# Performance work log

Hardware: AMD Instinct MI355X
Metric: run time of the kernel (lower is better)

## Reference

```python
import jax, jax.numpy as jnp
import numpy as np

B, T = 128, 1024
SERIES_IN, Y = 35, 8
H = 256
CON, BIN = 25, 10
D = SERIES_IN + Y  # 43, lstm input size


def setup_inputs() -> dict:
    key = jax.random.key(0)
    ks = jax.random.split(key, 14)
    def w(k, shape, s=0.05):
        return jax.random.normal(k, shape, dtype=jnp.float32) * s
    return {
        "x": jax.random.normal(ks[0], (B, T, D), dtype=jnp.float32),
        # DPLSTM (single layer), gate order i,f,g,o like torch
        "W_ih": w(ks[1], (4 * H, D)),
        "W_hh": w(ks[2], (4 * H, H)),
        "b_ih": w(ks[3], (4 * H,)),
        "b_hh": w(ks[4], (4 * H,)),
        # action head
        "W_afc1": w(ks[5], (H, H)),
        "b_afc1": w(ks[6], (H,)),
        "W_aout": w(ks[7], (Y, H)),
        "b_aout": w(ks[8], (Y,)),
        # outcome heads take [out, current_action] -> H+Y features
        "W_cont": w(ks[9], (2 * CON, H + Y)),
        "b_cont": w(ks[10], (2 * CON,)),
        "W_bin": w(ks[11], (BIN, H + Y)),
        "b_bin": w(ks[12], (BIN,)),
    }


def lstm(x, W_ih, W_hh, b_ih, b_hh):
    # x: [B, T, D] -> hidden states [B, T, H]; torch gate order i, f, g, o
    Hh = W_hh.shape[1]
    # precompute input projections for all timesteps (fold both biases in)
    xg = jnp.einsum("btd,gd->btg", x, W_ih) + b_ih + b_hh  # [B, T, 4H]

    def step(carry, g_t):
        h, c = carry
        gates = g_t + h @ W_hh.T  # [B, 4H]
        i, f, g, o = jnp.split(gates, 4, axis=-1)
        i = jax.nn.sigmoid(i)
        f = jax.nn.sigmoid(f)
        g = jnp.tanh(g)
        o = jax.nn.sigmoid(o)
        c = f * c + i * g
        h = o * jnp.tanh(c)
        return (h, c), h

    Bsz = x.shape[0]
    init = (jnp.zeros((Bsz, Hh), x.dtype), jnp.zeros((Bsz, Hh), x.dtype))
    _, hs = jax.lax.scan(step, init, jnp.swapaxes(xg, 0, 1))  # [T, B, H]
    return jnp.swapaxes(hs, 0, 1)


def reference(x, W_ih, W_hh, b_ih, b_hh, W_afc1, b_afc1, W_aout, b_aout,
              W_cont, b_cont, W_bin, b_bin):
    cur = x[:, :, -Y:]                                   # current action [B,T,Y]
    prev = jnp.concatenate([jnp.zeros_like(cur[:, :1]), cur[:, :-1]], axis=1)
    xin = jnp.concatenate([x[:, :, :-Y], prev], axis=-1)  # [B,T,D]
    out = lstm(xin, W_ih, W_hh, b_ih, b_hh)               # [B,T,H]
    # gradient reversal is identity in forward
    act = jax.nn.relu(out @ W_afc1.T + b_afc1) @ W_aout.T + b_aout  # [B,T,Y]
    pred = jnp.concatenate([out, cur], axis=-1)           # [B,T,H+Y]
    cont_params = pred @ W_cont.T + b_cont                # [B,T,2*CON]
    bin_params = jax.nn.sigmoid(pred @ W_bin.T + b_bin)   # [B,T,BIN]
    return cont_params, bin_params, act
```

## Files before the change

kernel.cpp:

```cpp
#include <hip/hip_runtime.h>

typedef unsigned int u32;
typedef unsigned short u16;
typedef unsigned char u8;
typedef unsigned long long u64;
typedef __attribute__((ext_vector_type(8))) short short8;
typedef __attribute__((ext_vector_type(4))) float floatx4;
typedef __attribute__((ext_vector_type(4))) int intx4;

#define TT 1024
#define BIN_OFF 6553600
#define ACT_OFF 7864320

__device__ __forceinline__ u16 f2b(float f) {
  u32 u = __builtin_bit_cast(u32, f);
  u += 0x7fffu + ((u >> 16) & 1u);
  return (u16)(u >> 16);
}
__device__ __forceinline__ float sigm2(float z) {
  return __builtin_amdgcn_rcpf(1.0f + __expf(-z));
}
__device__ __forceinline__ float tanh2(float z) {
  z = fminf(z, 15.0f);
  float e = __expf(2.0f * z);
  return (e - 1.0f) * __builtin_amdgcn_rcpf(e + 1.0f);
}
__device__ __forceinline__ float sigmf(float x) { return 1.0f / (1.0f + __expf(-x)); }


__global__ void k_zero4(u32* __restrict__ p) {
  if (threadIdx.x < 4) p[threadIdx.x] = 0;
}
__global__ void k_amax(const float* __restrict__ x, const float* __restrict__ wih,
                       const float* __restrict__ whh, u32* __restrict__ am) {
  __shared__ float red[256];
  const int tid = threadIdx.x;
  int b = blockIdx.x;
  const float* src; size_t n; int sec, b0, nb;
  if (b < 1920)      { src = x;   n = 5636096; sec = 0; b0 = 0;    nb = 1920; }
  else if (b < 2016) { src = whh; n = 262144;  sec = 1; b0 = 1920; nb = 96; }
  else               { src = wih; n = 44032;   sec = 2; b0 = 2016; nb = 32; }
  float m = 0.f;
  for (size_t i = (size_t)(b - b0) * 256 + tid; i < n; i += (size_t)nb * 256)
    m = fmaxf(m, fabsf(src[i]));
  red[tid] = m;
  __syncthreads();
  for (int s = 128; s > 0; s >>= 1) {
    if (tid < s) red[tid] = fmaxf(red[tid], red[tid + s]);
    __syncthreads();
  }
  if (tid == 0) atomicMax(&am[sec], __float_as_uint(red[0]));
}
__global__ void k_prep_bias(const float* __restrict__ a, const float* __restrict__ b,
                            float* __restrict__ o) {
  int i = blockIdx.x * 256 + threadIdx.x;
  o[i] = a[i] + b[i];
}
__global__ void k_prep_wq2(const float* __restrict__ wih, const float* __restrict__ whh,
                           const float* __restrict__ bias, const u32* __restrict__ am,
                           int* __restrict__ wq, float* __restrict__ sbuf) {
  u32 idx = blockIdx.x * 256 + threadIdx.x;
  const float xmax = fmaxf(__uint_as_float(am[0]), 1e-8f);
  const float whm  = fmaxf(__uint_as_float(am[1]), 1e-8f);
  const float wxm  = fmaxf(__uint_as_float(am[2]), 1e-8f);
  const float sn_h = whm / 127.0f, sn_x = wxm / 127.0f;
  const float sx = xmax / 127.0f;
  const float A_h = sn_h / 127.0f;
  const float A_x = sn_x * sx;
  if (idx == 0) { sbuf[0] = A_h; sbuf[1] = A_x; }
  int jq = idx & 3;
  int lane = (idx >> 2) & 63;
  u32 wf = idx >> 8;
  int F = wf % 40, w = wf / 40;
  int tile = F / 5, c = F % 5;
  int gate = tile >> 1, ht = tile & 1;
  int l15 = lane & 15, kq = lane >> 4;
  int n = gate * 256 + w * 32 + ht * 16 + l15;
  u32 out = 0;
#pragma unroll
  for (int b = 0; b < 4; ++b) {
    int kl = kq * 16 + jq * 4 + b;
    float q = 0.f;
    if (c < 4) {
      q = rintf(whh[n * 256 + c * 64 + kl] / sn_h);
    } else {
      if (kl < 43) q = rintf(wih[n * 43 + kl] / sn_x);
      else if (kl == 43) {
        q = fminf(fmaxf(rintf(bias[n] / (127.0f * A_x)), -127.f), 127.f);
      } else if (kl == 44) {
        float qc = fminf(fmaxf(rintf(bias[n] / (127.0f * A_x)), -127.f), 127.f);
        q = rintf((bias[n] - qc * 127.0f * A_x) / (127.0f * A_h));
      }
    }
    q = fminf(fmaxf(q, -127.f), 127.f);
    int qi = (int)q;
    out |= ((u32)(qi & 255)) << (8 * b);
  }
  wq[idx] = (int)out;
}
__global__ void k_prep_xq2(const float* __restrict__ x, const u32* __restrict__ am,
                           int* __restrict__ xq) {
  u32 idx = blockIdx.x * 256 + threadIdx.x;
  const float xmax = fmaxf(__uint_as_float(am[0]), 1e-8f);
  const float whm  = fmaxf(__uint_as_float(am[1]), 1e-8f);
  const float wxm  = fmaxf(__uint_as_float(am[2]), 1e-8f);
  const float sx = xmax / 127.0f;
  const float sr = whm / (127.0f * wxm);
  u32 unit = idx >> 8;
  u32 dwIn = idx & 255;
  int lane = dwIn >> 2, reg = dwIn & 3;
  int m = lane & 15, kq = lane >> 4;
  int bg = unit >> 8;
  int rem = unit & 255;
  int mt = rem >> 1, res = rem & 1;
  int t = mt * 8 + (m >> 1);
  int row = bg * 2 + (m & 1);
  u32 out = 0;
#pragma unroll
  for (int b = 0; b < 4; ++b) {
    int k = kq * 16 + reg * 4 + b;
    int q = 0;
    if (k < 43) {
      float xv = 0.f;
      if (k < 35) xv = x[((size_t)row * TT + t) * 43 + k];
      else if (t > 0) xv = x[((size_t)row * TT + (t - 1)) * 43 + k];
      float q1 = fminf(fmaxf(rintf(xv / sx), -127.f), 127.f);
      if (!res) q = (int)q1;
      else q = (int)fminf(fmaxf(rintf((xv - sx * q1) / sr), -127.f), 127.f);
    } else if (k == 43) q = res ? 0 : 127;
    else if (k == 44) q = res ? 127 : 0;
    out |= ((u32)(q & 255)) << (8 * b);
  }
  xq[idx] = (int)out;
}
__global__ void k_prep_afc(const float* __restrict__ wafc1, const float* __restrict__ waout,
                           u16* __restrict__ ob1, u16* __restrict__ ob2) {
  int r = blockIdx.x, k = threadIdx.x;
  if (r < 256) ob1[r * 256 + k] = f2b(wafc1[r * 256 + k]);
  else {
    int y = r - 256;
    ob2[y * 256 + k] = f2b(y < 8 ? waout[y * 256 + k] : 0.f);
  }
}
__global__ void k_prep_wcb(const float* __restrict__ wcont, const float* __restrict__ wbin,
                           u16* __restrict__ o) {
  int nrow = blockIdx.x, k = threadIdx.x;
  float v = 0.f;
  if (k < 264) {
    if (nrow < 50) v = wcont[nrow * 264 + k];
    else if (nrow < 60) v = wbin[(nrow - 50) * 264 + k];
  }
  o[nrow * 288 + k] = f2b(v);
}

#define XS 257
#define BARX() do { \
  asm volatile("s_waitcnt lgkmcnt(0)" ::: "memory"); \
  __builtin_amdgcn_s_barrier(); \
  __builtin_amdgcn_sched_barrier(0); \
} while (0)
#define PHASEG_HALF(xgw, HT, XM, XR) do { \
  const intx4 z_ = {0, 0, 0, 0}; \
  intx4 AX_[4], AR_[4]; \
  _Pragma("unroll") \
  for (int g_ = 0; g_ < 4; ++g_) { \
    const int F_ = (g_ * 2 + (HT)) * 5 + 4; \
    AX_[g_] = __builtin_amdgcn_mfma_i32_16x16x64_i8(wfr[F_], (XM), z_, 0, 0, 0); \
    AR_[g_] = __builtin_amdgcn_mfma_i32_16x16x64_i8(wfr[F_], (XR), z_, 0, 0, 0); \
  } \
  _Pragma("unroll") \
  for (int rr_ = 0; rr_ < 4; ++rr_) { \
    floatx4 P_; \
    _Pragma("unroll") \
    for (int g_ = 0; g_ < 4; ++g_) \
      P_[g_] = A_x * (float)AX_[g_][rr_] + A_h * (float)AR_[g_][rr_]; \
    (xgw)[l15 * XS + wcol + (HT) * 16 + rr_] = P_; \
  } \
} while (0)

__global__ __launch_bounds__(512, 1)
void k_scan12(const int* wq_, const int* __restrict__ xqd,
              const float* __restrict__ sb, u16* __restrict__ hs) {
  __shared__ u8 bimg[2 * 4096];
  __shared__ intx4 gimg[2 * XS];
  __shared__ floatx4 xg[2][16 * XS];
  const int tid = threadIdx.x;
  const int w = tid >> 6, lane = tid & 63;
  const int l15 = lane & 15, kq = lane >> 4;
  const int bg = blockIdx.x;

  *(uint4*)&bimg[tid * 16] = (uint4){0, 0, 0, 0};

  intx4 wfr[40];
  {
    const intx4* wp = (const intx4*)wq_ + (size_t)(w * 40) * 64 + lane;
#pragma unroll
    for (int F = 0; F < 40; ++F) wfr[F] = wp[(size_t)F * 64];
  }
  const float A_h = sb[0], A_x = sb[1];

  const int* xu = xqd + (size_t)bg * 65536;
  const int wcol = w * 32 + kq * 4;
  const int lr = lane >> 5, lc = lane & 31;
  const int mycol = w * 32 + lc;
  const int bwr = lr * 256 + (((mycol >> 4) ^ lr) << 4) + (mycol & 15);
  u16* hgp = hs + ((size_t)(bg * 2 + lr) * TT) * 256 + mycol;

  {
    intx4 xcm = *(const intx4*)(xu + lane * 4);
    intx4 xcr = *(const intx4*)(xu + 256 + lane * 4);
    PHASEG_HALF(xg[0], 0, xcm, xcr);
    PHASEG_HALF(xg[0], 1, xcm, xcr);
  }
  intx4 xnm = *(const intx4*)(xu + 512 + lane * 4);
  intx4 xnr = *(const intx4*)(xu + 512 + 256 + lane * 4);

  float c_st = 0.f;
  u16 h16 = 0;
  __syncthreads();

  int t = 0;
  for (int ch = 0; ch < 128; ++ch) {
    const int rb = ch & 1, wb = rb ^ 1;
#pragma unroll 1
    for (int tl = 0; tl < 8; ++tl, ++t) {
      const int cur = t & 1, nxt = cur ^ 1;
      if (t > 0) hgp[(size_t)(t - 1) * 256] = h16;
      intx4 bh[4];
#pragma unroll
      for (int c = 0; c < 4; ++c)
        bh[c] = *(const intx4*)&bimg[cur * 4096 + l15 * 256 +
                                     ((((c * 4 + kq) ^ l15) & 15) << 4)];
      floatx4 P = xg[rb][(tl * 2 + lr) * XS + mycol];
      const intx4 z = {0, 0, 0, 0};
      __builtin_amdgcn_s_setprio(1);
#pragma unroll
      for (int ht = 0; ht < 2; ++ht) {
        intx4 A[4];
#pragma unroll
        for (int g = 0; g < 4; ++g) {
          const int F = (g * 2 + ht) * 5;
          intx4 a = __builtin_amdgcn_mfma_i32_16x16x64_i8(wfr[F + 0], bh[0], z, 0, 0, 0);
          a = __builtin_amdgcn_mfma_i32_16x16x64_i8(wfr[F + 1], bh[1], a, 0, 0, 0);
          a = __builtin_amdgcn_mfma_i32_16x16x64_i8(wfr[F + 2], bh[2], a, 0, 0, 0);
          A[g] = __builtin_amdgcn_mfma_i32_16x16x64_i8(wfr[F + 3], bh[3], a, 0, 0, 0);
        }
        if (l15 < 2) {
#pragma unroll
          for (int rr = 0; rr < 4; ++rr) {
            intx4 v = {A[0][rr], A[1][rr], A[2][rr], A[3][rr]};
            gimg[l15 * XS + wcol + ht * 16 + rr] = v;
          }
        }
      }
      __builtin_amdgcn_s_setprio(0);
      asm volatile("s_waitcnt lgkmcnt(0)" ::: "memory");
      __builtin_amdgcn_sched_barrier(0);
      intx4 ah = gimg[lr * XS + mycol];
      float iv = sigm2(fmaf(A_h, (float)ah[0], P[0]));
      float fv = sigm2(fmaf(A_h, (float)ah[1], P[1]));
      float gv = tanh2(fmaf(A_h, (float)ah[2], P[2]));
      float ov = sigm2(fmaf(A_h, (float)ah[3], P[3]));
      float cc = fv * c_st + iv * gv;
      c_st = cc;
      float h = ov * tanh2(cc);
      int q = (int)rintf(h * 127.0f);
      bimg[nxt * 4096 + bwr] = (u8)q;
      h16 = f2b(h);
      if (tl == 0)      PHASEG_HALF(xg[wb], 0, xnm, xnr);
      else if (tl == 1) PHASEG_HALF(xg[wb], 1, xnm, xnr);
      else if (tl == 2) {
        const int chn = ch + 2 < 128 ? ch + 2 : 127;
        xnm = *(const intx4*)(xu + chn * 512 + lane * 4);
        xnr = *(const intx4*)(xu + chn * 512 + 256 + lane * 4);
      }
      BARX();
    }
  }
  hgp[(size_t)(TT - 1) * 256] = h16;
}


__global__ __launch_bounds__(256, 2)
void k_act(const u16* __restrict__ hs, const u16* __restrict__ wafc1,
           const u16* __restrict__ waout, const float* __restrict__ b_afc1,
           const float* __restrict__ b_aout, float* __restrict__ act) {
  __shared__ u16 a_sh[16 * 264];
  __shared__ u16 z_sh[16 * 264];
  __shared__ float sb1[256];
  const int tid = threadIdx.x;
  const int wave = tid >> 6, lane = tid & 63;
  const int l15 = lane & 15, kq = lane >> 4;
  const size_t bt0 = (size_t)blockIdx.x * 16;
  sb1[tid] = b_afc1[tid];
#pragma unroll
  for (int i = 0; i < 2; ++i) {
    int chunk = i * 256 + tid;
    int row = chunk >> 5, c = chunk & 31;
    *(uint4*)&a_sh[row * 264 + c * 8] = *(const uint4*)(hs + (bt0 + row) * 256 + c * 8);
  }
  __syncthreads();
  floatx4 acc[4];
#pragma unroll
  for (int nt = 0; nt < 4; ++nt) acc[nt] = (floatx4){0.f, 0.f, 0.f, 0.f};
#pragma unroll
  for (int kt = 0; kt < 8; ++kt) {
    short8 a = *(const short8*)&a_sh[l15 * 264 + kt * 32 + kq * 8];
#pragma unroll
    for (int nt = 0; nt < 4; ++nt) {
      int n = wave * 64 + nt * 16 + l15;
      short8 b = *(const short8*)(wafc1 + n * 256 + kt * 32 + kq * 8);
      acc[nt] = __builtin_amdgcn_mfma_f32_16x16x32_bf16(a, b, acc[nt], 0, 0, 0);
    }
  }
#pragma unroll
  for (int nt = 0; nt < 4; ++nt) {
    int n = wave * 64 + nt * 16 + l15;
    float bb = sb1[n];
#pragma unroll
    for (int r = 0; r < 4; ++r) {
      float v = acc[nt][r] + bb;
      v = v > 0.f ? v : 0.f;
      z_sh[(kq * 4 + r) * 264 + n] = f2b(v);
    }
  }
  __syncthreads();
  if (wave == 0) {
    floatx4 a2 = (floatx4){0.f, 0.f, 0.f, 0.f};
#pragma unroll
    for (int kt = 0; kt < 8; ++kt) {
      short8 a = *(const short8*)&z_sh[l15 * 264 + kt * 32 + kq * 8];
      short8 b = *(const short8*)(waout + l15 * 256 + kt * 32 + kq * 8);
      a2 = __builtin_amdgcn_mfma_f32_16x16x32_bf16(a, b, a2, 0, 0, 0);
    }
    if (l15 < 8) {
      float bb = b_aout[l15];
#pragma unroll
      for (int r = 0; r < 4; ++r)
        act[(bt0 + (size_t)(kq * 4 + r)) * 8 + l15] = a2[r] + bb;
    }
  }
}

__global__ __launch_bounds__(256, 2)
void k_cb(const u16* __restrict__ hs, const float* __restrict__ x,
          const u16* __restrict__ wcb, const float* __restrict__ b_cont,
          const float* __restrict__ b_bin, float* __restrict__ dout) {
  __shared__ u16 a_sh[16 * 296];
  const int tid = threadIdx.x;
  const int wave = tid >> 6, lane = tid & 63;
  const int l15 = lane & 15, kq = lane >> 4;
  const size_t bt0 = (size_t)blockIdx.x * 16;
#pragma unroll
  for (int i = 0; i < 2; ++i) {
    int chunk = i * 256 + tid;
    int row = chunk >> 5, c = chunk & 31;
    *(uint4*)&a_sh[row * 296 + c * 8] = *(const uint4*)(hs + (bt0 + row) * 256 + c * 8);
  }
  if (tid < 128) {
    int m = tid >> 3, j = tid & 7;
    a_sh[m * 296 + 256 + j] = f2b(x[(bt0 + m) * 43 + 35 + j]);
  }
  for (int i = tid; i < 384; i += 256) {
    int m = i / 24, jj = i % 24;
    a_sh[m * 296 + 264 + jj] = 0;
  }
  __syncthreads();
  const int n = wave * 16 + l15;
  floatx4 acc = (floatx4){0.f, 0.f, 0.f, 0.f};
#pragma unroll
  for (int kt = 0; kt < 9; ++kt) {
    short8 a = *(const short8*)&a_sh[l15 * 296 + kt * 32 + kq * 8];
    short8 b = *(const short8*)(wcb + n * 288 + kt * 32 + kq * 8);
    acc = __builtin_amdgcn_mfma_f32_16x16x32_bf16(a, b, acc, 0, 0, 0);
  }
  if (n < 50) {
    float bb = b_cont[n];
#pragma unroll
    for (int r = 0; r < 4; ++r)
      dout[(bt0 + (size_t)(kq * 4 + r)) * 50 + n] = acc[r] + bb;
  } else if (n < 60) {
    float bb = b_bin[n - 50];
#pragma unroll
    for (int r = 0; r < 4; ++r)
      dout[BIN_OFF + (bt0 + (size_t)(kq * 4 + r)) * 10 + (n - 50)] = sigmf(acc[r] + bb);
  }
}

extern "C" void kernel_launch(void* const* d_in, const int* in_sizes, int n_in,
                              void* d_out, int out_size, void* d_ws, size_t ws_size,
                              hipStream_t stream) {
  const float* x      = (const float*)d_in[0];
  const float* W_ih   = (const float*)d_in[1];
  const float* W_hh   = (const float*)d_in[2];
  const float* b_ih   = (const float*)d_in[3];
  const float* b_hh   = (const float*)d_in[4];
  const float* W_afc1 = (const float*)d_in[5];
  const float* b_afc1 = (const float*)d_in[6];
  const float* W_aout = (const float*)d_in[7];
  const float* b_aout = (const float*)d_in[8];
  const float* W_cont = (const float*)d_in[9];
  const float* b_cont = (const float*)d_in[10];
  const float* W_bin  = (const float*)d_in[11];
  const float* b_bin  = (const float*)d_in[12];
  float* outf = (float*)d_out;
  char* ws = (char*)d_ws;

  u32*   am     = (u32*)(ws);
  float* bias   = (float*)(ws + 64);
  float* sbuf   = (float*)(ws + 4160);
  int*   wq     = (int*)(ws + 4224);
  u16*   wafc1b = (u16*)(ws + 331904);
  u16*   waoutb = (u16*)(ws + 462976);
  u16*   wcbb   = (u16*)(ws + 471168);
  int*   xqd    = (int*)(ws + 524288);
  u16*   hs     = (u16*)(ws + 17305600);

  hipLaunchKernelGGL(k_zero4, dim3(1), dim3(64), 0, stream, am);
  hipLaunchKernelGGL(k_amax, dim3(2048), dim3(256), 0, stream, x, W_ih, W_hh, am);
  hipLaunchKernelGGL(k_prep_bias, dim3(4), dim3(256), 0, stream, b_ih, b_hh, bias);
  hipLaunchKernelGGL(k_prep_wq2, dim3(320), dim3(256), 0, stream, W_ih, W_hh, bias, am, wq, sbuf);
  hipLaunchKernelGGL(k_prep_xq2, dim3(16384), dim3(256), 0, stream, x, am, xqd);
  hipLaunchKernelGGL(k_prep_afc, dim3(272), dim3(256), 0, stream, W_afc1, W_aout, wafc1b, waoutb);
  hipLaunchKernelGGL(k_prep_wcb, dim3(64), dim3(288), 0, stream, W_cont, W_bin, wcbb);
  hipLaunchKernelGGL(k_scan12, dim3(64), dim3(512), 0, stream, wq, xqd, sbuf, hs);
  hipLaunchKernelGGL(k_act, dim3(8192), dim3(256), 0, stream, hs, wafc1b, waoutb, b_afc1, b_aout, outf + ACT_OFF);
  hipLaunchKernelGGL(k_cb, dim3(8192), dim3(256), 0, stream, hs, x, wcbb, b_cont, b_bin, outf);
}
```

Baseline: 1.387 ms.

## Halve scan block to 4 waves, each owning twice the hidden columns

The recurrent LSTM scan kernel now runs 256 threads (4 waves) per block instead of 512. Each wave holds 80 int8 weight fragments in registers instead of 40 and computes two hidden columns per lane. The gate-accumulator exchange is rewritten to a scalar-int LDS layout with per-gate rows, written directly after each MFMA chain. The intent is cheaper per-step barriers and fewer waves contending for sync. The cost is more serial MFMA work per wave and much higher register pressure, which risks spills.

```diff
diff --git a/kernel.cpp b/kernel.cpp
--- a/kernel.cpp
+++ b/kernel.cpp
@@ -154,17 +154,18 @@
 }
 
 #define XS 257
+#define GS 264
 #define BARX() do { \
   asm volatile("s_waitcnt lgkmcnt(0)" ::: "memory"); \
   __builtin_amdgcn_s_barrier(); \
   __builtin_amdgcn_sched_barrier(0); \
 } while (0)
-#define PHASEG_HALF(xgw, HT, XM, XR) do { \
+#define PHASEG_J(xgw, J, XM, XR) do { \
   const intx4 z_ = {0, 0, 0, 0}; \
   intx4 AX_[4], AR_[4]; \
   _Pragma("unroll") \
   for (int g_ = 0; g_ < 4; ++g_) { \
-    const int F_ = (g_ * 2 + (HT)) * 5 + 4; \
+    const int F_ = ((J) >> 1) * 40 + (g_ * 2 + ((J) & 1)) * 5 + 4; \
     AX_[g_] = __builtin_amdgcn_mfma_i32_16x16x64_i8(wfr[F_], (XM), z_, 0, 0, 0); \
     AR_[g_] = __builtin_amdgcn_mfma_i32_16x16x64_i8(wfr[F_], (XR), z_, 0, 0, 0); \
   } \
@@ -174,49 +175,52 @@
     _Pragma("unroll") \
     for (int g_ = 0; g_ < 4; ++g_) \
       P_[g_] = A_x * (float)AX_[g_][rr_] + A_h * (float)AR_[g_][rr_]; \
-    (xgw)[l15 * XS + wcol + (HT) * 16 + rr_] = P_; \
+    (xgw)[l15 * XS + w * 64 + (J) * 16 + kq * 4 + rr_] = P_; \
   } \
 } while (0)
 
-__global__ __launch_bounds__(512, 1)
-void k_scan12(const int* wq_, const int* __restrict__ xqd,
+__global__ __launch_bounds__(256, 1)
+void k_scan13(const int* wq_, const int* __restrict__ xqd,
               const float* __restrict__ sb, u16* __restrict__ hs) {
   __shared__ u8 bimg[2 * 4096];
-  __shared__ intx4 gimg[2 * XS];
+  __shared__ int gimg[8 * GS];
   __shared__ floatx4 xg[2][16 * XS];
   const int tid = threadIdx.x;
   const int w = tid >> 6, lane = tid & 63;
   const int l15 = lane & 15, kq = lane >> 4;
   const int bg = blockIdx.x;
 
-  *(uint4*)&bimg[tid * 16] = (uint4){0, 0, 0, 0};
-
-  intx4 wfr[40];
+  *(uint4*)&bimg[tid * 32] = (uint4){0, 0, 0, 0};
+  *(uint4*)&bimg[tid * 32 + 16] = (uint4){0, 0, 0, 0};
+
+  intx4 wfr[80];
   {
-    const intx4* wp = (const intx4*)wq_ + (size_t)(w * 40) * 64 + lane;
-#pragma unroll
-    for (int F = 0; F < 40; ++F) wfr[F] = wp[(size_t)F * 64];
+    const intx4* wp = (const intx4*)wq_ + (size_t)(w * 80) * 64 + lane;
+#pragma unroll
+    for (int F = 0; F < 80; ++F) wfr[F] = wp[(size_t)F * 64];
   }
   const float A_h = sb[0], A_x = sb[1];
 
   const int* xu = xqd + (size_t)bg * 65536;
-  const int wcol = w * 32 + kq * 4;
   const int lr = lane >> 5, lc = lane & 31;
-  const int mycol = w * 32 + lc;
-  const int bwr = lr * 256 + (((mycol >> 4) ^ lr) << 4) + (mycol & 15);
-  u16* hgp = hs + ((size_t)(bg * 2 + lr) * TT) * 256 + mycol;
+  const int c0 = w * 64 + lc, c1 = c0 + 32;
+  const int bw0 = lr * 256 + (((c0 >> 4) ^ lr) << 4) + (c0 & 15);
+  const int bw1 = lr * 256 + (((c1 >> 4) ^ lr) << 4) + (c1 & 15);
+  u16* hgp = hs + ((size_t)(bg * 2 + lr) * TT) * 256;
 
   {
     intx4 xcm = *(const intx4*)(xu + lane * 4);
     intx4 xcr = *(const intx4*)(xu + 256 + lane * 4);
-    PHASEG_HALF(xg[0], 0, xcm, xcr);
-    PHASEG_HALF(xg[0], 1, xcm, xcr);
+    PHASEG_J(xg[0], 0, xcm, xcr);
+    PHASEG_J(xg[0], 1, xcm, xcr);
+    PHASEG_J(xg[0], 2, xcm, xcr);
+    PHASEG_J(xg[0], 3, xcm, xcr);
   }
   intx4 xnm = *(const intx4*)(xu + 512 + lane * 4);
   intx4 xnr = *(const intx4*)(xu + 512 + 256 + lane * 4);
 
-  float c_st = 0.f;
-  u16 h16 = 0;
+  float cs0 = 0.f, cs1 = 0.f;
+  u16 h0 = 0, h1 = 0;
   __syncthreads();
 
   int t = 0;
@@ -225,51 +229,66 @@
 #pragma unroll 1
     for (int tl = 0; tl < 8; ++tl, ++t) {
       const int cur = t & 1, nxt = cur ^ 1;
-      if (t > 0) hgp[(size_t)(t - 1) * 256] = h16;
+      if (t > 0) {
+        hgp[(size_t)(t - 1) * 256 + c0] = h0;
+        hgp[(size_t)(t - 1) * 256 + c1] = h1;
+      }
       intx4 bh[4];
 #pragma unroll
       for (int c = 0; c < 4; ++c)
         bh[c] = *(const intx4*)&bimg[cur * 4096 + l15 * 256 +
                                      ((((c * 4 + kq) ^ l15) & 15) << 4)];
-      floatx4 P = xg[rb][(tl * 2 + lr) * XS + mycol];
+      floatx4 P0 = xg[rb][(tl * 2 + lr) * XS + c0];
+      floatx4 P1 = xg[rb][(tl * 2 + lr) * XS + c1];
       const intx4 z = {0, 0, 0, 0};
       __builtin_amdgcn_s_setprio(1);
 #pragma unroll
-      for (int ht = 0; ht < 2; ++ht) {
-        intx4 A[4];
+      for (int j = 0; j < 4; ++j) {
 #pragma unroll
         for (int g = 0; g < 4; ++g) {
-          const int F = (g * 2 + ht) * 5;
+          const int F = (j >> 1) * 40 + (g * 2 + (j & 1)) * 5;
           intx4 a = __builtin_amdgcn_mfma_i32_16x16x64_i8(wfr[F + 0], bh[0], z, 0, 0, 0);
           a = __builtin_amdgcn_mfma_i32_16x16x64_i8(wfr[F + 1], bh[1], a, 0, 0, 0);
           a = __builtin_amdgcn_mfma_i32_16x16x64_i8(wfr[F + 2], bh[2], a, 0, 0, 0);
-          A[g] = __builtin_amdgcn_mfma_i32_16x16x64_i8(wfr[F + 3], bh[3], a, 0, 0, 0);
-        }
-        if (l15 < 2) {
-#pragma unroll
-          for (int rr = 0; rr < 4; ++rr) {
-            intx4 v = {A[0][rr], A[1][rr], A[2][rr], A[3][rr]};
-            gimg[l15 * XS + wcol + ht * 16 + rr] = v;
-          }
+          a = __builtin_amdgcn_mfma_i32_16x16x64_i8(wfr[F + 3], bh[3], a, 0, 0, 0);
+          if (l15 < 2)
+            *(intx4*)&gimg[(l15 * 4 + g) * GS + w * 64 + j * 16 + kq * 4] = a;
         }
       }
       __builtin_amdgcn_s_setprio(0);
       asm volatile("s_waitcnt lgkmcnt(0)" ::: "memory");
       __builtin_amdgcn_sched_barrier(0);
-      intx4 ah = gimg[lr * XS + mycol];
-      float iv = sigm2(fmaf(A_h, (float)ah[0], P[0]));
-      float fv = sigm2(fmaf(A_h, (float)ah[1], P[1]));
-      float gv = tanh2(fmaf(A_h, (float)ah[2], P[2]));
-      float ov = sigm2(fmaf(A_h, (float)ah[3], P[3]));
-      float cc = fv * c_st + iv * gv;
-      c_st = cc;
-      float h = ov * tanh2(cc);
-      int q = (int)rintf(h * 127.0f);
-      bimg[nxt * 4096 + bwr] = (u8)q;
-      h16 = f2b(h);
-      if (tl == 0)      PHASEG_HALF(xg[wb], 0, xnm, xnr);
-      else if (tl == 1) PHASEG_HALF(xg[wb], 1, xnm, xnr);
-      else if (tl == 2) {
+      float a00 = (float)gimg[(lr * 4 + 0) * GS + c0];
+      float a01 = (float)gimg[(lr * 4 + 1) * GS + c0];
+      float a02 = (float)gimg[(lr * 4 + 2) * GS + c0];
+      float a03 = (float)gimg[(lr * 4 + 3) * GS + c0];
+      float a10 = (float)gimg[(lr * 4 + 0) * GS + c1];
+      float a11 = (float)gimg[(lr * 4 + 1) * GS + c1];
+      float a12 = (float)gimg[(lr * 4 + 2) * GS + c1];
+      float a13 = (float)gimg[(lr * 4 + 3) * GS + c1];
+      float iv0 = sigm2(fmaf(A_h, a00, P0[0]));
+      float fv0 = sigm2(fmaf(A_h, a01, P0[1]));
+      float gv0 = tanh2(fmaf(A_h, a02, P0[2]));
+      float ov0 = sigm2(fmaf(A_h, a03, P0[3]));
+      float cc0 = fv0 * cs0 + iv0 * gv0;
+      cs0 = cc0;
+      float hh0 = ov0 * tanh2(cc0);
+      float iv1 = sigm2(fmaf(A_h, a10, P1[0]));
+      float fv1 = sigm2(fmaf(A_h, a11, P1[1]));
+      float gv1 = tanh2(fmaf(A_h, a12, P1[2]));
+      float ov1 = sigm2(fmaf(A_h, a13, P1[3]));
+      float cc1 = fv1 * cs1 + iv1 * gv1;
+      cs1 = cc1;
+      float hh1 = ov1 * tanh2(cc1);
+      bimg[nxt * 4096 + bw0] = (u8)(int)rintf(hh0 * 127.0f);
+      bimg[nxt * 4096 + bw1] = (u8)(int)rintf(hh1 * 127.0f);
+      h0 = f2b(hh0);
+      h1 = f2b(hh1);
+      if (tl == 0)      PHASEG_J(xg[wb], 0, xnm, xnr);
+      else if (tl == 1) PHASEG_J(xg[wb], 1, xnm, xnr);
+      else if (tl == 2) PHASEG_J(xg[wb], 2, xnm, xnr);
+      else if (tl == 3) PHASEG_J(xg[wb], 3, xnm, xnr);
+      else if (tl == 4) {
         const int chn = ch + 2 < 128 ? ch + 2 : 127;
         xnm = *(const intx4*)(xu + chn * 512 + lane * 4);
         xnr = *(const intx4*)(xu + chn * 512 + 256 + lane * 4);
@@ -277,7 +296,8 @@
       BARX();
     }
   }
-  hgp[(size_t)(TT - 1) * 256] = h16;
+  hgp[(size_t)(TT - 1) * 256 + c0] = h0;
+  hgp[(size_t)(TT - 1) * 256 + c1] = h1;
 }
 
 
@@ -423,7 +443,7 @@
   hipLaunchKernelGGL(k_prep_xq2, dim3(16384), dim3(256), 0, stream, x, am, xqd);
   hipLaunchKernelGGL(k_prep_afc, dim3(272), dim3(256), 0, stream, W_afc1, W_aout, wafc1b, waoutb);
   hipLaunchKernelGGL(k_prep_wcb, dim3(64), dim3(288), 0, stream, W_cont, W_bin, wcbb);
-  hipLaunchKernelGGL(k_scan12, dim3(64), dim3(512), 0, stream, wq, xqd, sbuf, hs);
+  hipLaunchKernelGGL(k_scan13, dim3(64), dim3(256), 0, stream, wq, xqd, sbuf, hs);
   hipLaunchKernelGGL(k_act, dim3(8192), dim3(256), 0, stream, hs, wafc1b, waoutb, b_afc1, b_aout, outf + ACT_OFF);
   hipLaunchKernelGGL(k_cb, dim3(8192), dim3(256), 0, stream, hs, x, wcbb, b_cont, b_bin, outf);
 }
```

Measured after the change: 1.892 ms. 36.4% more time.

## Fold log2e into gate scales, unroll scan steps, transpose gate exchange layout

Applied to the files above, without the earlier changes.

The input projection and recurrent scale factors now carry log2(e) (and 2*log2(e) for the g gate), so the gate activations use exp2f directly without an extra multiply. The 8-step inner loop is fully unrolled with compile-time buffer indices and precomputed LDS addresses. The gate exchange buffer in shared memory changes from interleaved intx4 to per-gate planar rows, so each MFMA accumulator is stored as one vector and read back as scalars. These steps aim to shorten the serial per-timestep critical path of the LSTM scan, at the cost of more code size and register pressure.

```diff
diff --git a/kernel.cpp b/kernel.cpp
--- a/kernel.cpp
+++ b/kernel.cpp
@@ -16,14 +16,6 @@
   u32 u = __builtin_bit_cast(u32, f);
   u += 0x7fffu + ((u >> 16) & 1u);
   return (u16)(u >> 16);
-}
-__device__ __forceinline__ float sigm2(float z) {
-  return __builtin_amdgcn_rcpf(1.0f + __expf(-z));
-}
-__device__ __forceinline__ float tanh2(float z) {
-  z = fminf(z, 15.0f);
-  float e = __expf(2.0f * z);
-  return (e - 1.0f) * __builtin_amdgcn_rcpf(e + 1.0f);
 }
 __device__ __forceinline__ float sigmf(float x) { return 1.0f / (1.0f + __expf(-x)); }
 
@@ -154,35 +146,99 @@
 }
 
 #define XS 257
+#define GS2 264
 #define BARX() do { \
   asm volatile("s_waitcnt lgkmcnt(0)" ::: "memory"); \
   __builtin_amdgcn_s_barrier(); \
   __builtin_amdgcn_sched_barrier(0); \
 } while (0)
-#define PHASEG_HALF(xgw, HT, XM, XR) do { \
-  const intx4 z_ = {0, 0, 0, 0}; \
-  intx4 AX_[4], AR_[4]; \
-  _Pragma("unroll") \
-  for (int g_ = 0; g_ < 4; ++g_) { \
-    const int F_ = (g_ * 2 + (HT)) * 5 + 4; \
-    AX_[g_] = __builtin_amdgcn_mfma_i32_16x16x64_i8(wfr[F_], (XM), z_, 0, 0, 0); \
-    AR_[g_] = __builtin_amdgcn_mfma_i32_16x16x64_i8(wfr[F_], (XR), z_, 0, 0, 0); \
+
+template <int HT>
+__device__ __forceinline__ void phaseg(const intx4 (&wfr)[40], intx4 xm, intx4 xr,
+                                       floatx4* xgw, int l15, int wcol,
+                                       float Sx1, float Sx2, float Ah1, float Ah2) {
+  const intx4 z = {0, 0, 0, 0};
+  intx4 AX[4], AR[4];
+#pragma unroll
+  for (int g = 0; g < 4; ++g) {
+    const int F = (g * 2 + HT) * 5 + 4;
+    AX[g] = __builtin_amdgcn_mfma_i32_16x16x64_i8(wfr[F], xm, z, 0, 0, 0);
+    AR[g] = __builtin_amdgcn_mfma_i32_16x16x64_i8(wfr[F], xr, z, 0, 0, 0);
+  }
+#pragma unroll
+  for (int rr = 0; rr < 4; ++rr) {
+    floatx4 P;
+#pragma unroll
+    for (int g = 0; g < 4; ++g) {
+      const float sx = (g == 2) ? Sx2 : Sx1;
+      const float sh = (g == 2) ? Ah2 : Ah1;
+      P[g] = fmaf(sx, (float)AX[g][rr], sh * (float)AR[g][rr]);
+    }
+    xgw[l15 * XS + wcol + HT * 16 + rr] = P;
+  }
+}
+
+#define MCH(DST, G, HT) { \
+  const int F_ = ((G) * 2 + (HT)) * 5; \
+  intx4 a_ = __builtin_amdgcn_mfma_i32_16x16x64_i8(wfr[F_ + 0], bh0, z, 0, 0, 0); \
+  a_ = __builtin_amdgcn_mfma_i32_16x16x64_i8(wfr[F_ + 1], bh1, a_, 0, 0, 0); \
+  a_ = __builtin_amdgcn_mfma_i32_16x16x64_i8(wfr[F_ + 2], bh2, a_, 0, 0, 0); \
+  DST = __builtin_amdgcn_mfma_i32_16x16x64_i8(wfr[F_ + 3], bh3, a_, 0, 0, 0); \
+}
+
+#define STEP(TL, EXTRA) do { \
+  enum { CUR = (TL) & 1, NXT = CUR ^ 1 }; \
+  if ((TL) == 0) { if (ch > 0) hb[-256] = h16; } \
+  else hb[((TL) - 1) * 256] = h16; \
+  intx4 bh0 = *(const intx4*)&bimg[CUR * 4096 + bA0]; \
+  intx4 bh1 = *(const intx4*)&bimg[CUR * 4096 + bA1]; \
+  intx4 bh2 = *(const intx4*)&bimg[CUR * 4096 + bA2]; \
+  intx4 bh3 = *(const intx4*)&bimg[CUR * 4096 + bA3]; \
+  floatx4 P = xgr[((TL) * 2 + lr) * XS + mycol]; \
+  const intx4 z = {0, 0, 0, 0}; \
+  intx4 A0, A1, A2, A3, A4, A5, A6, A7; \
+  __builtin_amdgcn_s_setprio(1); \
+  MCH(A0, 0, 0) MCH(A1, 1, 0) MCH(A2, 2, 0) MCH(A3, 3, 0) \
+  MCH(A4, 0, 1) MCH(A5, 1, 1) MCH(A6, 2, 1) MCH(A7, 3, 1) \
+  __builtin_amdgcn_s_setprio(0); \
+  if (l15 < 2) { \
+    *(intx4*)&gw[0 * GS2 +  0] = A0; *(intx4*)&gw[1 * GS2 +  0] = A1; \
+    *(intx4*)&gw[2 * GS2 +  0] = A2; *(intx4*)&gw[3 * GS2 +  0] = A3; \
+    *(intx4*)&gw[0 * GS2 + 16] = A4; *(intx4*)&gw[1 * GS2 + 16] = A5; \
+    *(intx4*)&gw[2 * GS2 + 16] = A6; *(intx4*)&gw[3 * GS2 + 16] = A7; \
   } \
-  _Pragma("unroll") \
-  for (int rr_ = 0; rr_ < 4; ++rr_) { \
-    floatx4 P_; \
-    _Pragma("unroll") \
-    for (int g_ = 0; g_ < 4; ++g_) \
-      P_[g_] = A_x * (float)AX_[g_][rr_] + A_h * (float)AR_[g_][rr_]; \
-    (xgw)[l15 * XS + wcol + (HT) * 16 + rr_] = P_; \
+  asm volatile("s_waitcnt lgkmcnt(0)" ::: "memory"); \
+  __builtin_amdgcn_sched_barrier(0); \
+  { \
+    float a0 = (float)gr[0 * GS2], a1 = (float)gr[1 * GS2]; \
+    float a2 = (float)gr[2 * GS2], a3 = (float)gr[3 * GS2]; \
+    float zz0 = fmaf(Ah1, a0, P[0]); \
+    float zz1 = fmaf(Ah1, a1, P[1]); \
+    float zz2 = fminf(fmaf(Ah2, a2, P[2]), 43.0f); \
+    float zz3 = fmaf(Ah1, a3, P[3]); \
+    float iv = __builtin_amdgcn_rcpf(1.0f + exp2f(-zz0)); \
+    float fv = __builtin_amdgcn_rcpf(1.0f + exp2f(-zz1)); \
+    float eg = exp2f(zz2); \
+    float gv = (eg - 1.0f) * __builtin_amdgcn_rcpf(eg + 1.0f); \
+    float ov = __builtin_amdgcn_rcpf(1.0f + exp2f(-zz3)); \
+    float cc = fv * c_st + iv * gv; \
+    c_st = cc; \
+    float dd = fminf(cc * T2L2E, 43.0f); \
+    float ec = exp2f(dd); \
+    float th = (ec - 1.0f) * __builtin_amdgcn_rcpf(ec + 1.0f); \
+    float h = ov * th; \
+    bimg[NXT * 4096 + bw0] = (u8)(int)rintf(h * 127.0f); \
+    h16 = f2b(h); \
   } \
+  EXTRA \
+  BARX(); \
 } while (0)
 
 __global__ __launch_bounds__(512, 1)
-void k_scan12(const int* wq_, const int* __restrict__ xqd,
+void k_scan14(const int* wq_, const int* __restrict__ xqd,
               const float* __restrict__ sb, u16* __restrict__ hs) {
   __shared__ u8 bimg[2 * 4096];
-  __shared__ intx4 gimg[2 * XS];
+  __shared__ int gimg[8 * GS2];
   __shared__ floatx4 xg[2][16 * XS];
   const int tid = threadIdx.x;
   const int w = tid >> 6, lane = tid & 63;
@@ -197,20 +253,30 @@
 #pragma unroll
     for (int F = 0; F < 40; ++F) wfr[F] = wp[(size_t)F * 64];
   }
+  const float L2E = 1.44269504f;
   const float A_h = sb[0], A_x = sb[1];
+  const float Ah1 = A_h * L2E, Ah2 = A_h * 2.0f * L2E;
+  const float Sx1 = A_x * L2E, Sx2 = A_x * 2.0f * L2E;
+  const float T2L2E = 2.0f * L2E;
 
   const int* xu = xqd + (size_t)bg * 65536;
   const int wcol = w * 32 + kq * 4;
   const int lr = lane >> 5, lc = lane & 31;
   const int mycol = w * 32 + lc;
-  const int bwr = lr * 256 + (((mycol >> 4) ^ lr) << 4) + (mycol & 15);
+  const int bw0 = lr * 256 + (((mycol >> 4) ^ lr) << 4) + (mycol & 15);
+  const int bA0 = l15 * 256 + ((((0 * 4 + kq) ^ l15) & 15) << 4);
+  const int bA1 = l15 * 256 + ((((1 * 4 + kq) ^ l15) & 15) << 4);
+  const int bA2 = l15 * 256 + ((((2 * 4 + kq) ^ l15) & 15) << 4);
+  const int bA3 = l15 * 256 + ((((3 * 4 + kq) ^ l15) & 15) << 4);
+  int* gw = &gimg[(l15 * 4) * GS2 + w * 32 + kq * 4];
+  const int* gr = &gimg[(lr * 4) * GS2 + mycol];
   u16* hgp = hs + ((size_t)(bg * 2 + lr) * TT) * 256 + mycol;
 
   {
     intx4 xcm = *(const intx4*)(xu + lane * 4);
     intx4 xcr = *(const intx4*)(xu + 256 + lane * 4);
-    PHASEG_HALF(xg[0], 0, xcm, xcr);
-    PHASEG_HALF(xg[0], 1, xcm, xcr);
+    phaseg<0>(wfr, xcm, xcr, xg[0], l15, wcol, Sx1, Sx2, Ah1, Ah2);
+    phaseg<1>(wfr, xcm, xcr, xg[0], l15, wcol, Sx1, Sx2, Ah1, Ah2);
   }
   intx4 xnm = *(const intx4*)(xu + 512 + lane * 4);
   intx4 xnr = *(const intx4*)(xu + 512 + 256 + lane * 4);
@@ -219,63 +285,21 @@
   u16 h16 = 0;
   __syncthreads();
 
-  int t = 0;
   for (int ch = 0; ch < 128; ++ch) {
-    const int rb = ch & 1, wb = rb ^ 1;
-#pragma unroll 1
-    for (int tl = 0; tl < 8; ++tl, ++t) {
-      const int cur = t & 1, nxt = cur ^ 1;
-      if (t > 0) hgp[(size_t)(t - 1) * 256] = h16;
-      intx4 bh[4];
-#pragma unroll
-      for (int c = 0; c < 4; ++c)
-        bh[c] = *(const intx4*)&bimg[cur * 4096 + l15 * 256 +
-                                     ((((c * 4 + kq) ^ l15) & 15) << 4)];
-      floatx4 P = xg[rb][(tl * 2 + lr) * XS + mycol];
-      const intx4 z = {0, 0, 0, 0};
-      __builtin_amdgcn_s_setprio(1);
-#pragma unroll
-      for (int ht = 0; ht < 2; ++ht) {
-        intx4 A[4];
-#pragma unroll
-        for (int g = 0; g < 4; ++g) {
-          const int F = (g * 2 + ht) * 5;
-          intx4 a = __builtin_amdgcn_mfma_i32_16x16x64_i8(wfr[F + 0], bh[0], z, 0, 0, 0);
-          a = __builtin_amdgcn_mfma_i32_16x16x64_i8(wfr[F + 1], bh[1], a, 0, 0, 0);
-          a = __builtin_amdgcn_mfma_i32_16x16x64_i8(wfr[F + 2], bh[2], a, 0, 0, 0);
-          A[g] = __builtin_amdgcn_mfma_i32_16x16x64_i8(wfr[F + 3], bh[3], a, 0, 0, 0);
-        }
-        if (l15 < 2) {
-#pragma unroll
-          for (int rr = 0; rr < 4; ++rr) {
-            intx4 v = {A[0][rr], A[1][rr], A[2][rr], A[3][rr]};
-            gimg[l15 * XS + wcol + ht * 16 + rr] = v;
-          }
-        }
-      }
-      __builtin_amdgcn_s_setprio(0);
-      asm volatile("s_waitcnt lgkmcnt(0)" ::: "memory");
-      __builtin_amdgcn_sched_barrier(0);
-      intx4 ah = gimg[lr * XS + mycol];
-      float iv = sigm2(fmaf(A_h, (float)ah[0], P[0]));
-      float fv = sigm2(fmaf(A_h, (float)ah[1], P[1]));
-      float gv = tanh2(fmaf(A_h, (float)ah[2], P[2]));
-      float ov = sigm2(fmaf(A_h, (float)ah[3], P[3]));
-      float cc = fv * c_st + iv * gv;
-      c_st = cc;
-      float h = ov * tanh2(cc);
-      int q = (int)rintf(h * 127.0f);
-      bimg[nxt * 4096 + bwr] = (u8)q;
-      h16 = f2b(h);
-      if (tl == 0)      PHASEG_HALF(xg[wb], 0, xnm, xnr);
-      else if (tl == 1) PHASEG_HALF(xg[wb], 1, xnm, xnr);
-      else if (tl == 2) {
-        const int chn = ch + 2 < 128 ? ch + 2 : 127;
-        xnm = *(const intx4*)(xu + chn * 512 + lane * 4);
-        xnr = *(const intx4*)(xu + chn * 512 + 256 + lane * 4);
-      }
-      BARX();
-    }
+    const int rb = ch & 1;
+    const floatx4* xgr = xg[rb];
+    floatx4* xgw2 = xg[rb ^ 1];
+    u16* hb = hgp + (size_t)ch * 2048;
+    STEP(0, phaseg<0>(wfr, xnm, xnr, xgw2, l15, wcol, Sx1, Sx2, Ah1, Ah2););
+    STEP(1, phaseg<1>(wfr, xnm, xnr, xgw2, l15, wcol, Sx1, Sx2, Ah1, Ah2););
+    STEP(2, { const int chn = ch + 2 < 128 ? ch + 2 : 127;
+              xnm = *(const intx4*)(xu + chn * 512 + lane * 4);
+              xnr = *(const intx4*)(xu + chn * 512 + 256 + lane * 4); });
+    STEP(3, ;);
+    STEP(4, ;);
+    STEP(5, ;);
+    STEP(6, ;);
+    STEP(7, ;);
   }
   hgp[(size_t)(TT - 1) * 256] = h16;
 }
@@ -423,7 +447,7 @@
   hipLaunchKernelGGL(k_prep_xq2, dim3(16384), dim3(256), 0, stream, x, am, xqd);
   hipLaunchKernelGGL(k_prep_afc, dim3(272), dim3(256), 0, stream, W_afc1, W_aout, wafc1b, waoutb);
   hipLaunchKernelGGL(k_prep_wcb, dim3(64), dim3(288), 0, stream, W_cont, W_bin, wcbb);
-  hipLaunchKernelGGL(k_scan12, dim3(64), dim3(512), 0, stream, wq, xqd, sbuf, hs);
+  hipLaunchKernelGGL(k_scan14, dim3(64), dim3(512), 0, stream, wq, xqd, sbuf, hs);
   hipLaunchKernelGGL(k_act, dim3(8192), dim3(256), 0, stream, hs, wafc1b, waoutb, b_afc1, b_aout, outf + ACT_OFF);
   hipLaunchKernelGGL(k_cb, dim3(8192), dim3(256), 0, stream, hs, x, wcbb, b_cont, b_bin, outf);
 }
```

Result: faster. 1.328 ms (-4.3%).
